# Kernel tuning notes

Measured on AMD Instinct MI355X. Metric: run time of the kernel, lower is better.

Reference implementation:

```python
import jax, jax.numpy as jnp
import numpy as np

EMBED = 1024
HEADS = 16
HEAD_DIM = EMBED // HEADS


def setup_inputs() -> dict:
    key = jax.random.key(0)
    ks = jax.random.split(key, 6)
    N, S = 4, 1024
    query = jax.random.normal(ks[0], (N, S, EMBED), dtype=jnp.float32)
    keys = jax.random.normal(ks[1], (N, S, EMBED), dtype=jnp.float32)
    values = jax.random.normal(ks[2], (N, S, EMBED), dtype=jnp.float32)
    mask = jax.random.randint(ks[3], (N, 1, S, S), 0, 2, dtype=jnp.int32)
    W_out = jax.random.normal(ks[4], (EMBED, EMBED), dtype=jnp.float32) * (1.0 / np.sqrt(EMBED))
    b_out = jax.random.normal(ks[5], (EMBED,), dtype=jnp.float32) * 0.02
    return {"query": query, "keys": keys, "values": values, "mask": mask,
            "W_out": W_out, "b_out": b_out}


def reference(query, keys, values, mask, W_out, b_out):
    N, Q, _ = query.shape
    K = keys.shape[1]
    # NOTE: the torch module never applies its per-head q/k/v Linear layers;
    # only the reshape + attention + fc_out are in the forward path.
    q = query.reshape(N, Q, HEADS, HEAD_DIM)
    k = keys.reshape(N, K, HEADS, HEAD_DIM)
    v = values.reshape(N, K, HEADS, HEAD_DIM)
    # energy: [N, H, Q, K]
    energy = jnp.einsum("bqhd,bkhd->bhqk", q, k)
    energy = jnp.where(mask == 0, jnp.float32(-1e20), energy)
    attn = jax.nn.softmax(energy / jnp.sqrt(jnp.float32(HEAD_DIM)), axis=3)
    out = jnp.einsum("bhqk,bkhd->bqhd", attn, v).reshape(N, Q, HEADS * HEAD_DIM)
    return out @ W_out.T + b_out
```

## Files before the change

### kernel.cpp

```cpp
#include <hip/hip_runtime.h>
#include <math.h>

#define NB 4
#define SL 1024
#define EMB 1024
#define NH 16
#define HD 64
#define QB 128

typedef __attribute__((ext_vector_type(8))) short bf16x8;
typedef __attribute__((ext_vector_type(4))) float f32x4;
typedef __attribute__((ext_vector_type(4))) unsigned u32x4;

static __device__ __forceinline__ unsigned pk2(float a, float b) {
    unsigned x = __float_as_uint(a) + 0x8000u;
    unsigned y = __float_as_uint(b) + 0x8000u;
    return (x >> 16) | (y & 0xFFFF0000u);
}
static __device__ __forceinline__ float exp2_fast(float x) {
    float r; asm("v_exp_f32 %0, %1" : "=v"(r) : "v"(x)); return r;
}
static __device__ __forceinline__ void gload_lds16(const void* g, void* l) {
    __builtin_amdgcn_global_load_lds(
        (const __attribute__((address_space(1))) unsigned int*)g,
        (__attribute__((address_space(3))) unsigned int*)l, 16, 0, 0);
}

#define VMW(n) asm volatile("s_waitcnt vmcnt(" #n ")" ::: "memory")
#define MEMPIN() asm volatile("" ::: "memory")

__global__ __launch_bounds__(256) void prep(
    const float* __restrict__ W, unsigned short* __restrict__ Wb,
    const float* __restrict__ Kf, unsigned short* __restrict__ Kb,
    const float* __restrict__ V, unsigned short* __restrict__ Vt,
    const int* __restrict__ mask, unsigned long long* __restrict__ Mbt,
    const float* __restrict__ Qf, unsigned short* __restrict__ Qb)
{
    __shared__ unsigned short sT[128 * 68];
    const int bid = blockIdx.x, tid = threadIdx.x;

    if (bid < 512) {
        int i = (bid * 256 + tid) * 8;
        float4 f0 = *(const float4*)&W[i];
        float4 f1 = *(const float4*)&W[i + 4];
        uint4 u = { pk2(f0.x,f0.y), pk2(f0.z,f0.w), pk2(f1.x,f1.y), pk2(f1.z,f1.w) };
        *(uint4*)&Wb[i] = u;
    } else if (bid < 2560) {
        int t = bid - 512;
        int b = t >> 9, h = (t >> 5) & 15, k0 = (t & 31) * 32;
        int r = tid >> 3, d = (tid & 7) * 8;
        const float* gp = &Kf[((size_t)(b * SL + k0 + r)) * EMB + h * HD + d];
        float4 f0 = *(const float4*)gp, f1 = *(const float4*)(gp + 4);
        uint4 u = { pk2(f0.x,f0.y), pk2(f0.z,f0.w), pk2(f1.x,f1.y), pk2(f1.z,f1.w) };
        *(uint4*)&Kb[((size_t)((b * NH + h) * SL + k0 + r)) * HD + d] = u;
    } else if (bid < 3072) {
        int t = bid - 2560;
        int bh = t >> 3, kb = t & 7;
        int b = bh >> 4, h = bh & 15;
        int k0 = kb * 128;
        #pragma unroll
        for (int i = 0; i < 4; ++i) {
            int lin = (i * 256 + tid) * 8;
            int r = lin >> 6, d = lin & 63;
            const float* gp = &V[((size_t)(b * SL + k0 + r)) * EMB + h * HD + d];
            float4 f0 = *(const float4*)gp, f1 = *(const float4*)(gp + 4);
            uint2 u0 = { pk2(f0.x,f0.y), pk2(f0.z,f0.w) };
            uint2 u1 = { pk2(f1.x,f1.y), pk2(f1.z,f1.w) };
            *(uint2*)&sT[r * 68 + d]     = u0;
            *(uint2*)&sT[r * 68 + d + 4] = u1;
        }
        __syncthreads();
        #pragma unroll
        for (int p = 0; p < 4; ++p) {
            int d = p * 16 + (tid >> 4);
            int c = tid & 15;
            unsigned v[4];
            #pragma unroll
            for (int j = 0; j < 4; ++j) {
                unsigned lo = sT[(c * 8 + 2 * j) * 68 + d];
                unsigned hi = sT[(c * 8 + 2 * j + 1) * 68 + d];
                v[j] = lo | (hi << 16);
            }
            uint4 u = { v[0], v[1], v[2], v[3] };
            *(uint4*)&Vt[((size_t)(bh * HD + d)) * SL + k0 + c * 8] = u;
        }
    } else if (bid < 7168) {
        int t = bid - 3072;
        int lane = tid & 63;
        #pragma unroll
        for (int r = 0; r < 4; ++r) {
            int wid = (t * 4 + (tid >> 6)) * 4 + r;
            int c = wid & 15, q = (wid >> 4) & 1023, bb = wid >> 14;
            int mv = mask[((size_t)bb * SL + q) * SL + c * 64 + lane];
            unsigned long long bits = __ballot(mv != 0);
            if (lane == 0) Mbt[((size_t)bb * 16 + c) * SL + q] = bits;
        }
    } else {
        int t = bid - 7168;
        int b = t >> 9, h = (t >> 5) & 15, q0 = (t & 31) * 32;
        int r = tid >> 3, d = (tid & 7) * 8;
        const float* gp = &Qf[((size_t)(b * SL + q0 + r)) * EMB + h * HD + d];
        float4 f0 = *(const float4*)gp, f1 = *(const float4*)(gp + 4);
        uint4 u = { pk2(f0.x,f0.y), pk2(f0.z,f0.w), pk2(f1.x,f1.y), pk2(f1.z,f1.w) };
        *(uint4*)&Qb[((size_t)((b * NH + h) * SL + q0 + r)) * HD + d] = u;
    }
}

__global__ __launch_bounds__(256, 2) void attn_mfma(
    const unsigned short* __restrict__ Qb, const unsigned short* __restrict__ Kb,
    const unsigned short* __restrict__ Vt,
    const unsigned long long* __restrict__ Mbt,
    unsigned short* __restrict__ Oa)
{
    const int lin = blockIdx.x;
    const int xcd = lin & 7, slot = lin >> 3;
    const int bh = xcd * 8 + (slot >> 3);
    const int q0 = (slot & 7) * QB;
    const int b = bh >> 4, h = bh & 15;
    const int tid = threadIdx.x;
    const int w = tid >> 6, lane = tid & 63;
    const int m16 = lane & 15, quad = lane >> 4;
    const int lr = lane >> 3, lc = lane & 7;

    __shared__ __align__(16) unsigned short sK[3][64 * 64];
    __shared__ __align__(16) unsigned short sVt[3][64 * 64];

    const size_t vbase = (size_t)(bh * HD) * SL;
    const size_t kbase = (size_t)(bh * SL) * HD;
    const size_t mbase = (size_t)(b * 16) * SL + q0 + w * 32 + m16;
    const size_t qrowb = (size_t)(bh * SL + q0 + w * 32);

    bf16x8 bQ[2][2];
    #pragma unroll
    for (int u = 0; u < 2; ++u)
        #pragma unroll
        for (int hh = 0; hh < 2; ++hh)
            bQ[u][hh] = *(const bf16x8*)&Qb[(qrowb + u * 16 + m16) * HD + hh * 32 + quad * 8];
    MEMPIN();
    unsigned long long mbA0, mbA1, mbB0, mbB1, mbC0 = 0, mbC1 = 0;
    #pragma unroll
    for (int i = 0; i < 2; ++i) {
        int row = w * 16 + i * 8;
        gload_lds16(&Vt[vbase + (size_t)(row + lr) * SL + (lc ^ lr) * 8], &sVt[0][row * 64]);
        gload_lds16(&Kb[kbase + (size_t)(row + lr) * HD + (lc ^ lr) * 8], &sK[0][row * 64]);
    }
    MEMPIN();
    mbA0 = Mbt[mbase];
    mbA1 = Mbt[mbase + 16];
    MEMPIN();
    #pragma unroll
    for (int i = 0; i < 2; ++i) {
        int row = w * 16 + i * 8;
        gload_lds16(&Vt[vbase + (size_t)(row + lr) * SL + 64 + (lc ^ lr) * 8], &sVt[1][row * 64]);
        gload_lds16(&Kb[kbase + (size_t)(64 + row + lr) * HD + (lc ^ lr) * 8], &sK[1][row * 64]);
    }
    MEMPIN();
    mbB0 = Mbt[mbase + SL];
    mbB1 = Mbt[mbase + SL + 16];
    MEMPIN();

    unsigned short* kc = (unsigned short*)sK[0];
    unsigned short* kn = (unsigned short*)sK[1];
    unsigned short* k2 = (unsigned short*)sK[2];
    unsigned short* vc = (unsigned short*)sVt[0];
    unsigned short* vn = (unsigned short*)sVt[1];
    unsigned short* v2 = (unsigned short*)sVt[2];

    f32x4 O[2][4] = {};
    f32x4 lacc[2] = {};
    const float CSC = 0.125f * 1.44269504f;
    const short one_bf = (short)0x3F80;
    const bf16x8 ones = { one_bf, one_bf, one_bf, one_bf, one_bf, one_bf, one_bf, one_bf };

    for (int kt = 0; kt < 16; ++kt) {
        if (kt < 15) { VMW(8); } else { VMW(2); }
        __builtin_amdgcn_s_barrier();
        __builtin_amdgcn_sched_barrier(0);

        if (kt < 14) {
            const int k0n = (kt + 2) * 64;
            #pragma unroll
            for (int i = 0; i < 2; ++i) {
                int row = w * 16 + i * 8;
                gload_lds16(&Vt[vbase + (size_t)(row + lr) * SL + k0n + (lc ^ lr) * 8],
                            &v2[row * 64]);
                gload_lds16(&Kb[kbase + (size_t)(k0n + row + lr) * HD + (lc ^ lr) * 8],
                            &k2[row * 64]);
            }
            MEMPIN();
            mbC0 = Mbt[mbase + (size_t)(kt + 2) * SL];
            mbC1 = Mbt[mbase + (size_t)(kt + 2) * SL + 16];
            MEMPIN();
        }

        f32x4 sc[2][4];
        __builtin_amdgcn_s_setprio(1);
        #pragma unroll
        for (int t = 0; t < 4; ++t) {
            int krow = t * 16 + m16;
            bf16x8 a0 = *(const bf16x8*)&kc[krow * 64 + ((quad ^ (krow & 7)) * 8)];
            bf16x8 a1 = *(const bf16x8*)&kc[krow * 64 + (((4 + quad) ^ (krow & 7)) * 8)];
            f32x4 z = {0.f, 0.f, 0.f, 0.f};
            sc[0][t] = __builtin_amdgcn_mfma_f32_16x16x32_bf16(a0, bQ[0][0], z,        0,0,0);
            sc[0][t] = __builtin_amdgcn_mfma_f32_16x16x32_bf16(a1, bQ[0][1], sc[0][t], 0,0,0);
            sc[1][t] = __builtin_amdgcn_mfma_f32_16x16x32_bf16(a0, bQ[1][0], z,        0,0,0);
            sc[1][t] = __builtin_amdgcn_mfma_f32_16x16x32_bf16(a1, bQ[1][1], sc[1][t], 0,0,0);
        }
        __builtin_amdgcn_s_setprio(0);

        bf16x8 bP[2][2];
        #pragma unroll
        for (int u = 0; u < 2; ++u) {
            unsigned long long mb = u ? mbA1 : mbA0;
            unsigned mlo = (unsigned)mb, mhi = (unsigned)(mb >> 32);
            unsigned s0 = mlo >> (quad * 8);
            unsigned s1 = mhi >> (quad * 8);
            unsigned wt[4][2];
            #pragma unroll
            for (int t = 0; t < 4; ++t) {
                wt[t][0] = pk2(exp2_fast(sc[u][t][0] * CSC), exp2_fast(sc[u][t][1] * CSC));
                wt[t][1] = pk2(exp2_fast(sc[u][t][2] * CSC), exp2_fast(sc[u][t][3] * CSC));
            }
            unsigned g[2][4];
            #pragma unroll
            for (int hh = 0; hh < 2; ++hh)
                #pragma unroll
                for (int p = 0; p < 2; ++p) {
                    unsigned A = wt[2 * hh][p], B = wt[2 * hh + 1][p];
                    asm("v_permlane32_swap_b32 %0, %1" : "+v"(A), "+v"(B));
                    asm("v_permlane16_swap_b32 %0, %1" : "+v"(A), "+v"(B));
                    g[hh][p] = A; g[hh][2 + p] = B;
                }
            #pragma unroll
            for (int hh = 0; hh < 2; ++hh) {
                unsigned sb = hh ? s1 : s0;
                #pragma unroll
                for (int j2 = 0; j2 < 4; ++j2) {
                    unsigned b2 = (sb >> (2 * j2)) & 3u;
                    unsigned am = ((b2 & 1u) ? 0xFFFFu : 0u) | ((b2 & 2u) ? 0xFFFF0000u : 0u);
                    g[hh][j2] &= am;
                }
            }
            u32x4 p0 = { g[0][0], g[0][1], g[0][2], g[0][3] };
            u32x4 p1 = { g[1][0], g[1][1], g[1][2], g[1][3] };
            bP[u][0] = __builtin_bit_cast(bf16x8, p0);
            bP[u][1] = __builtin_bit_cast(bf16x8, p1);
        }

        __builtin_amdgcn_s_setprio(1);
        lacc[0] = __builtin_amdgcn_mfma_f32_16x16x32_bf16(ones, bP[0][0], lacc[0], 0,0,0);
        lacc[0] = __builtin_amdgcn_mfma_f32_16x16x32_bf16(ones, bP[0][1], lacc[0], 0,0,0);
        lacc[1] = __builtin_amdgcn_mfma_f32_16x16x32_bf16(ones, bP[1][0], lacc[1], 0,0,0);
        lacc[1] = __builtin_amdgcn_mfma_f32_16x16x32_bf16(ones, bP[1][1], lacc[1], 0,0,0);

        #pragma unroll
        for (int dt = 0; dt < 4; ++dt) {
            int drow = dt * 16 + m16;
            bf16x8 v0 = *(const bf16x8*)&vc[drow * 64 + ((quad ^ (drow & 7)) * 8)];
            bf16x8 v1 = *(const bf16x8*)&vc[drow * 64 + (((4 + quad) ^ (drow & 7)) * 8)];
            O[0][dt] = __builtin_amdgcn_mfma_f32_16x16x32_bf16(v0, bP[0][0], O[0][dt], 0,0,0);
            O[0][dt] = __builtin_amdgcn_mfma_f32_16x16x32_bf16(v1, bP[0][1], O[0][dt], 0,0,0);
            O[1][dt] = __builtin_amdgcn_mfma_f32_16x16x32_bf16(v0, bP[1][0], O[1][dt], 0,0,0);
            O[1][dt] = __builtin_amdgcn_mfma_f32_16x16x32_bf16(v1, bP[1][1], O[1][dt], 0,0,0);
        }
        __builtin_amdgcn_s_setprio(0);

        unsigned short* tk = kc; kc = kn; kn = k2; k2 = tk;
        unsigned short* tv = vc; vc = vn; vn = v2; v2 = tv;
        mbA0 = mbB0; mbA1 = mbB1; mbB0 = mbC0; mbB1 = mbC1;
    }

    #pragma unroll
    for (int u = 0; u < 2; ++u) {
        float inv = 1.f / lacc[u][0];
        size_t base = ((size_t)(b * SL + q0 + w * 32 + u * 16 + m16)) * EMB + h * HD + quad * 4;
        #pragma unroll
        for (int dt = 0; dt < 4; ++dt) {
            uint2 ow = { pk2(O[u][dt][0] * inv, O[u][dt][1] * inv),
                         pk2(O[u][dt][2] * inv, O[u][dt][3] * inv) };
            *(uint2*)&Oa[base + dt * 16] = ow;
        }
    }
}

__global__ __launch_bounds__(512, 2) void proj_mfma(
    const unsigned short* __restrict__ A, const unsigned short* __restrict__ Wb,
    const float* __restrict__ bias, float* __restrict__ C)
{
    const int n0 = blockIdx.x * 128;
    const int m0 = blockIdx.y * 128;
    const int tid = threadIdx.x;
    const int w = tid >> 6, lane = tid & 63;
    const int m16 = lane & 15, quad = lane >> 4;
    const int lr = lane >> 3, lc = lane & 7;
    const int wm = (w >> 2) * 64, wn = (w & 3) * 32;

    __shared__ __align__(16) unsigned short sA[2][128 * 64];
    __shared__ __align__(16) unsigned short sW[2][128 * 64];

    f32x4 acc[4][2] = {};

    #pragma unroll
    for (int i = 0; i < 2; ++i) {
        int r = w * 16 + i * 8;
        gload_lds16(&A [(size_t)(m0 + r + lr) * EMB + (lc ^ lr) * 8], &sA[0][r * 64]);
        gload_lds16(&Wb[(size_t)(n0 + r + lr) * EMB + (lc ^ lr) * 8], &sW[0][r * 64]);
    }
    __syncthreads();

    for (int it = 0; it < 16; ++it) {
        const int bf = it & 1;
        if (it < 15) {
            int e0 = (it + 1) * 64;
            #pragma unroll
            for (int i = 0; i < 2; ++i) {
                int r = w * 16 + i * 8;
                gload_lds16(&A [(size_t)(m0 + r + lr) * EMB + e0 + (lc ^ lr) * 8], &sA[bf ^ 1][r * 64]);
                gload_lds16(&Wb[(size_t)(n0 + r + lr) * EMB + e0 + (lc ^ lr) * 8], &sW[bf ^ 1][r * 64]);
            }
        }
        #pragma unroll
        for (int hh = 0; hh < 2; ++hh) {
            bf16x8 af[4], bw[2];
            #pragma unroll
            for (int mt = 0; mt < 4; ++mt) {
                int r = wm + mt * 16 + m16;
                af[mt] = *(const bf16x8*)&sA[bf][r * 64 + (((hh * 4 + quad) ^ (r & 7)) * 8)];
            }
            #pragma unroll
            for (int nt = 0; nt < 2; ++nt) {
                int r = wn + nt * 16 + m16;
                bw[nt] = *(const bf16x8*)&sW[bf][r * 64 + (((hh * 4 + quad) ^ (r & 7)) * 8)];
            }
            #pragma unroll
            for (int mt = 0; mt < 4; ++mt)
                #pragma unroll
                for (int nt = 0; nt < 2; ++nt)
                    acc[mt][nt] = __builtin_amdgcn_mfma_f32_16x16x32_bf16(af[mt], bw[nt], acc[mt][nt], 0,0,0);
        }
        __syncthreads();
    }

    #pragma unroll
    for (int nt = 0; nt < 2; ++nt) {
        float bv = bias[n0 + wn + nt * 16 + m16];
        #pragma unroll
        for (int mt = 0; mt < 4; ++mt) {
            size_t row = (size_t)(m0 + wm + mt * 16 + quad * 4);
            #pragma unroll
            for (int rg = 0; rg < 4; ++rg)
                C[(row + rg) * EMB + n0 + wn + nt * 16 + m16] = acc[mt][nt][rg] + bv;
        }
    }
}

extern "C" void kernel_launch(void* const* d_in, const int* in_sizes, int n_in,
                              void* d_out, int out_size, void* d_ws, size_t ws_size,
                              hipStream_t stream) {
    const float* Q    = (const float*)d_in[0];
    const float* K    = (const float*)d_in[1];
    const float* V    = (const float*)d_in[2];
    const int*   mask = (const int*)  d_in[3];
    const float* W    = (const float*)d_in[4];
    const float* bias = (const float*)d_in[5];

    unsigned short* Oa = (unsigned short*)d_ws;
    unsigned short* Wb = Oa + (size_t)NB * SL * EMB;
    unsigned long long* Mbt = (unsigned long long*)(Wb + (size_t)EMB * EMB);
    unsigned short* Vt = (unsigned short*)(Mbt + (size_t)NB * 16 * SL);
    unsigned short* Kb = Vt + (size_t)NB * NH * HD * SL;
    unsigned short* Qb = Kb + (size_t)NB * NH * SL * HD;

    prep<<<9216, 256, 0, stream>>>(W, Wb, K, Kb, V, Vt, mask, Mbt, Q, Qb);
    attn_mfma<<<512, 256, 0, stream>>>(Qb, Kb, Vt, Mbt, Oa);
    proj_mfma<<<dim3(EMB / 128, (NB * SL) / 128), 512, 0, stream>>>(Oa, Wb, bias, (float*)d_out);
}
```

Before: 167.5 us.

## Halve attention query tile and convert Q to bf16 inside attention kernel

The attention kernel now processes 64 query rows per block (16 per wave) instead of 128, doubling the grid to 1024 blocks and raising the occupancy hint to 3 blocks per CU. Q is read directly as fp32 and packed to bf16 in registers, which removes the Q conversion blocks from the prep kernel and the Qb workspace round trip. The trade-off is that each K/V tile loaded into LDS is now reused by half as many query rows, so total K/V traffic doubles. Each wave also has less MFMA work to hide load latency.

```diff
diff --git a/kernel.cpp b/kernel.cpp
--- a/kernel.cpp
+++ b/kernel.cpp
@@ -6,7 +6,7 @@
 #define EMB 1024
 #define NH 16
 #define HD 64
-#define QB 128
+#define QB 64
 
 typedef __attribute__((ext_vector_type(8))) short bf16x8;
 typedef __attribute__((ext_vector_type(4))) float f32x4;
@@ -33,8 +33,7 @@
     const float* __restrict__ W, unsigned short* __restrict__ Wb,
     const float* __restrict__ Kf, unsigned short* __restrict__ Kb,
     const float* __restrict__ V, unsigned short* __restrict__ Vt,
-    const int* __restrict__ mask, unsigned long long* __restrict__ Mbt,
-    const float* __restrict__ Qf, unsigned short* __restrict__ Qb)
+    const int* __restrict__ mask, unsigned long long* __restrict__ Mbt)
 {
     __shared__ unsigned short sT[128 * 68];
     const int bid = blockIdx.x, tid = threadIdx.x;
@@ -84,7 +83,7 @@
             uint4 u = { v[0], v[1], v[2], v[3] };
             *(uint4*)&Vt[((size_t)(bh * HD + d)) * SL + k0 + c * 8] = u;
         }
-    } else if (bid < 7168) {
+    } else {
         int t = bid - 3072;
         int lane = tid & 63;
         #pragma unroll
@@ -95,27 +94,19 @@
             unsigned long long bits = __ballot(mv != 0);
             if (lane == 0) Mbt[((size_t)bb * 16 + c) * SL + q] = bits;
         }
-    } else {
-        int t = bid - 7168;
-        int b = t >> 9, h = (t >> 5) & 15, q0 = (t & 31) * 32;
-        int r = tid >> 3, d = (tid & 7) * 8;
-        const float* gp = &Qf[((size_t)(b * SL + q0 + r)) * EMB + h * HD + d];
-        float4 f0 = *(const float4*)gp, f1 = *(const float4*)(gp + 4);
-        uint4 u = { pk2(f0.x,f0.y), pk2(f0.z,f0.w), pk2(f1.x,f1.y), pk2(f1.z,f1.w) };
-        *(uint4*)&Qb[((size_t)((b * NH + h) * SL + q0 + r)) * HD + d] = u;
-    }
-}
-
-__global__ __launch_bounds__(256, 2) void attn_mfma(
-    const unsigned short* __restrict__ Qb, const unsigned short* __restrict__ Kb,
+    }
+}
+
+__global__ __launch_bounds__(256, 3) void attn_mfma(
+    const float* __restrict__ Q, const unsigned short* __restrict__ Kb,
     const unsigned short* __restrict__ Vt,
     const unsigned long long* __restrict__ Mbt,
     unsigned short* __restrict__ Oa)
 {
     const int lin = blockIdx.x;
     const int xcd = lin & 7, slot = lin >> 3;
-    const int bh = xcd * 8 + (slot >> 3);
-    const int q0 = (slot & 7) * QB;
+    const int bh = xcd * 8 + (slot >> 4);
+    const int q0 = (slot & 15) * QB;
     const int b = bh >> 4, h = bh & 15;
     const int tid = threadIdx.x;
     const int w = tid >> 6, lane = tid & 63;
@@ -127,17 +118,20 @@
 
     const size_t vbase = (size_t)(bh * HD) * SL;
     const size_t kbase = (size_t)(bh * SL) * HD;
-    const size_t mbase = (size_t)(b * 16) * SL + q0 + w * 32 + m16;
-    const size_t qrowb = (size_t)(bh * SL + q0 + w * 32);
-
-    bf16x8 bQ[2][2];
-    #pragma unroll
-    for (int u = 0; u < 2; ++u)
-        #pragma unroll
-        for (int hh = 0; hh < 2; ++hh)
-            bQ[u][hh] = *(const bf16x8*)&Qb[(qrowb + u * 16 + m16) * HD + hh * 32 + quad * 8];
-    MEMPIN();
-    unsigned long long mbA0, mbA1, mbB0, mbB1, mbC0 = 0, mbC1 = 0;
+    const size_t mbase = (size_t)(b * 16) * SL + q0 + w * 16 + m16;
+
+    bf16x8 bQ[2];
+    {
+        const float* qp = &Q[((size_t)(b * SL + q0 + w * 16 + m16)) * EMB + h * HD + quad * 8];
+        float4 f0 = *(const float4*)qp,        f1 = *(const float4*)(qp + 4);
+        float4 f2 = *(const float4*)(qp + 32), f3 = *(const float4*)(qp + 36);
+        u32x4 u0 = { pk2(f0.x,f0.y), pk2(f0.z,f0.w), pk2(f1.x,f1.y), pk2(f1.z,f1.w) };
+        u32x4 u1 = { pk2(f2.x,f2.y), pk2(f2.z,f2.w), pk2(f3.x,f3.y), pk2(f3.z,f3.w) };
+        bQ[0] = __builtin_bit_cast(bf16x8, u0);
+        bQ[1] = __builtin_bit_cast(bf16x8, u1);
+    }
+    MEMPIN();
+    unsigned long long mbA, mbB, mbC = 0;
     #pragma unroll
     for (int i = 0; i < 2; ++i) {
         int row = w * 16 + i * 8;
@@ -145,8 +139,7 @@
         gload_lds16(&Kb[kbase + (size_t)(row + lr) * HD + (lc ^ lr) * 8], &sK[0][row * 64]);
     }
     MEMPIN();
-    mbA0 = Mbt[mbase];
-    mbA1 = Mbt[mbase + 16];
+    mbA = Mbt[mbase];
     MEMPIN();
     #pragma unroll
     for (int i = 0; i < 2; ++i) {
@@ -155,8 +148,7 @@
         gload_lds16(&Kb[kbase + (size_t)(64 + row + lr) * HD + (lc ^ lr) * 8], &sK[1][row * 64]);
     }
     MEMPIN();
-    mbB0 = Mbt[mbase + SL];
-    mbB1 = Mbt[mbase + SL + 16];
+    mbB = Mbt[mbase + SL];
     MEMPIN();
 
     unsigned short* kc = (unsigned short*)sK[0];
@@ -166,14 +158,14 @@
     unsigned short* vn = (unsigned short*)sVt[1];
     unsigned short* v2 = (unsigned short*)sVt[2];
 
-    f32x4 O[2][4] = {};
-    f32x4 lacc[2] = {};
+    f32x4 O[4] = {};
+    f32x4 lacc = {};
     const float CSC = 0.125f * 1.44269504f;
     const short one_bf = (short)0x3F80;
     const bf16x8 ones = { one_bf, one_bf, one_bf, one_bf, one_bf, one_bf, one_bf, one_bf };
 
     for (int kt = 0; kt < 16; ++kt) {
-        if (kt < 15) { VMW(8); } else { VMW(2); }
+        if (kt < 15) { VMW(5); } else { VMW(1); }
         __builtin_amdgcn_s_barrier();
         __builtin_amdgcn_sched_barrier(0);
 
@@ -188,12 +180,11 @@
                             &k2[row * 64]);
             }
             MEMPIN();
-            mbC0 = Mbt[mbase + (size_t)(kt + 2) * SL];
-            mbC1 = Mbt[mbase + (size_t)(kt + 2) * SL + 16];
+            mbC = Mbt[mbase + (size_t)(kt + 2) * SL];
             MEMPIN();
         }
 
-        f32x4 sc[2][4];
+        f32x4 sc[4];
         __builtin_amdgcn_s_setprio(1);
         #pragma unroll
         for (int t = 0; t < 4; ++t) {
@@ -201,25 +192,21 @@
             bf16x8 a0 = *(const bf16x8*)&kc[krow * 64 + ((quad ^ (krow & 7)) * 8)];
             bf16x8 a1 = *(const bf16x8*)&kc[krow * 64 + (((4 + quad) ^ (krow & 7)) * 8)];
             f32x4 z = {0.f, 0.f, 0.f, 0.f};
-            sc[0][t] = __builtin_amdgcn_mfma_f32_16x16x32_bf16(a0, bQ[0][0], z,        0,0,0);
-            sc[0][t] = __builtin_amdgcn_mfma_f32_16x16x32_bf16(a1, bQ[0][1], sc[0][t], 0,0,0);
-            sc[1][t] = __builtin_amdgcn_mfma_f32_16x16x32_bf16(a0, bQ[1][0], z,        0,0,0);
-            sc[1][t] = __builtin_amdgcn_mfma_f32_16x16x32_bf16(a1, bQ[1][1], sc[1][t], 0,0,0);
+            sc[t] = __builtin_amdgcn_mfma_f32_16x16x32_bf16(a0, bQ[0], z,     0,0,0);
+            sc[t] = __builtin_amdgcn_mfma_f32_16x16x32_bf16(a1, bQ[1], sc[t], 0,0,0);
         }
         __builtin_amdgcn_s_setprio(0);
 
-        bf16x8 bP[2][2];
-        #pragma unroll
-        for (int u = 0; u < 2; ++u) {
-            unsigned long long mb = u ? mbA1 : mbA0;
-            unsigned mlo = (unsigned)mb, mhi = (unsigned)(mb >> 32);
+        bf16x8 bP[2];
+        {
+            unsigned mlo = (unsigned)mbA, mhi = (unsigned)(mbA >> 32);
             unsigned s0 = mlo >> (quad * 8);
             unsigned s1 = mhi >> (quad * 8);
             unsigned wt[4][2];
             #pragma unroll
             for (int t = 0; t < 4; ++t) {
-                wt[t][0] = pk2(exp2_fast(sc[u][t][0] * CSC), exp2_fast(sc[u][t][1] * CSC));
-                wt[t][1] = pk2(exp2_fast(sc[u][t][2] * CSC), exp2_fast(sc[u][t][3] * CSC));
+                wt[t][0] = pk2(exp2_fast(sc[t][0] * CSC), exp2_fast(sc[t][1] * CSC));
+                wt[t][1] = pk2(exp2_fast(sc[t][2] * CSC), exp2_fast(sc[t][3] * CSC));
             }
             unsigned g[2][4];
             #pragma unroll
@@ -243,41 +230,36 @@
             }
             u32x4 p0 = { g[0][0], g[0][1], g[0][2], g[0][3] };
             u32x4 p1 = { g[1][0], g[1][1], g[1][2], g[1][3] };
-            bP[u][0] = __builtin_bit_cast(bf16x8, p0);
-            bP[u][1] = __builtin_bit_cast(bf16x8, p1);
+            bP[0] = __builtin_bit_cast(bf16x8, p0);
+            bP[1] = __builtin_bit_cast(bf16x8, p1);
         }
 
         __builtin_amdgcn_s_setprio(1);
-        lacc[0] = __builtin_amdgcn_mfma_f32_16x16x32_bf16(ones, bP[0][0], lacc[0], 0,0,0);
-        lacc[0] = __builtin_amdgcn_mfma_f32_16x16x32_bf16(ones, bP[0][1], lacc[0], 0,0,0);
-        lacc[1] = __builtin_amdgcn_mfma_f32_16x16x32_bf16(ones, bP[1][0], lacc[1], 0,0,0);
-        lacc[1] = __builtin_amdgcn_mfma_f32_16x16x32_bf16(ones, bP[1][1], lacc[1], 0,0,0);
+        lacc = __builtin_amdgcn_mfma_f32_16x16x32_bf16(ones, bP[0], lacc, 0,0,0);
+        lacc = __builtin_amdgcn_mfma_f32_16x16x32_bf16(ones, bP[1], lacc, 0,0,0);
 
         #pragma unroll
         for (int dt = 0; dt < 4; ++dt) {
             int drow = dt * 16 + m16;
             bf16x8 v0 = *(const bf16x8*)&vc[drow * 64 + ((quad ^ (drow & 7)) * 8)];
             bf16x8 v1 = *(const bf16x8*)&vc[drow * 64 + (((4 + quad) ^ (drow & 7)) * 8)];
-            O[0][dt] = __builtin_amdgcn_mfma_f32_16x16x32_bf16(v0, bP[0][0], O[0][dt], 0,0,0);
-            O[0][dt] = __builtin_amdgcn_mfma_f32_16x16x32_bf16(v1, bP[0][1], O[0][dt], 0,0,0);
-            O[1][dt] = __builtin_amdgcn_mfma_f32_16x16x32_bf16(v0, bP[1][0], O[1][dt], 0,0,0);
-            O[1][dt] = __builtin_amdgcn_mfma_f32_16x16x32_bf16(v1, bP[1][1], O[1][dt], 0,0,0);
+            O[dt] = __builtin_amdgcn_mfma_f32_16x16x32_bf16(v0, bP[0], O[dt], 0,0,0);
+            O[dt] = __builtin_amdgcn_mfma_f32_16x16x32_bf16(v1, bP[1], O[dt], 0,0,0);
         }
         __builtin_amdgcn_s_setprio(0);
 
         unsigned short* tk = kc; kc = kn; kn = k2; k2 = tk;
         unsigned short* tv = vc; vc = vn; vn = v2; v2 = tv;
-        mbA0 = mbB0; mbA1 = mbB1; mbB0 = mbC0; mbB1 = mbC1;
-    }
-
-    #pragma unroll
-    for (int u = 0; u < 2; ++u) {
-        float inv = 1.f / lacc[u][0];
-        size_t base = ((size_t)(b * SL + q0 + w * 32 + u * 16 + m16)) * EMB + h * HD + quad * 4;
+        mbA = mbB; mbB = mbC;
+    }
+
+    {
+        float inv = 1.f / lacc[0];
+        size_t base = ((size_t)(b * SL + q0 + w * 16 + m16)) * EMB + h * HD + quad * 4;
         #pragma unroll
         for (int dt = 0; dt < 4; ++dt) {
-            uint2 ow = { pk2(O[u][dt][0] * inv, O[u][dt][1] * inv),
-                         pk2(O[u][dt][2] * inv, O[u][dt][3] * inv) };
+            uint2 ow = { pk2(O[dt][0] * inv, O[dt][1] * inv),
+                         pk2(O[dt][2] * inv, O[dt][3] * inv) };
             *(uint2*)&Oa[base + dt * 16] = ow;
         }
     }
@@ -369,9 +351,8 @@
     unsigned long long* Mbt = (unsigned long long*)(Wb + (size_t)EMB * EMB);
     unsigned short* Vt = (unsigned short*)(Mbt + (size_t)NB * 16 * SL);
     unsigned short* Kb = Vt + (size_t)NB * NH * HD * SL;
-    unsigned short* Qb = Kb + (size_t)NB * NH * SL * HD;
-
-    prep<<<9216, 256, 0, stream>>>(W, Wb, K, Kb, V, Vt, mask, Mbt, Q, Qb);
-    attn_mfma<<<512, 256, 0, stream>>>(Qb, Kb, Vt, Mbt, Oa);
+
+    prep<<<7168, 256, 0, stream>>>(W, Wb, K, Kb, V, Vt, mask, Mbt);
+    attn_mfma<<<1024, 256, 0, stream>>>(Q, Kb, Vt, Mbt, Oa);
     proj_mfma<<<dim3(EMB / 128, (NB * SL) / 128), 512, 0, stream>>>(Oa, Wb, bias, (float*)d_out);
 }
```

New measurement: 169.6 us. About the same (+1.2%).

## Split key range across two wave groups, fuse Q conversion into attention

Applied to the files above, without the earlier changes.

The attention kernel now uses 512 threads. Two groups of four waves each process alternating 64-key tiles, and their partial O and row-sum accumulators are combined through LDS at the end. Q is loaded as fp32 and converted to bf16 inside the attention kernel, so the Q pass in prep is gone, and the softmax scale is folded into K during prep. Packing uses the hardware v_cvt_pk_bf16_f32 and a cheaper mask expansion. The pipeline is now a 4-slot buffer with a full vmcnt(0) wait every iteration. That wait and the final reduction could cut latency hiding, but the split gives more waves per block.

```diff
diff --git a/kernel.cpp b/kernel.cpp
--- a/kernel.cpp
+++ b/kernel.cpp
@@ -20,6 +20,9 @@
 static __device__ __forceinline__ float exp2_fast(float x) {
     float r; asm("v_exp_f32 %0, %1" : "=v"(r) : "v"(x)); return r;
 }
+static __device__ __forceinline__ unsigned cvtpk(float a, float b) {
+    unsigned r; asm("v_cvt_pk_bf16_f32 %0, %1, %2" : "=v"(r) : "v"(a), "v"(b)); return r;
+}
 static __device__ __forceinline__ void gload_lds16(const void* g, void* l) {
     __builtin_amdgcn_global_load_lds(
         (const __attribute__((address_space(1))) unsigned int*)g,
@@ -33,11 +36,11 @@
     const float* __restrict__ W, unsigned short* __restrict__ Wb,
     const float* __restrict__ Kf, unsigned short* __restrict__ Kb,
     const float* __restrict__ V, unsigned short* __restrict__ Vt,
-    const int* __restrict__ mask, unsigned long long* __restrict__ Mbt,
-    const float* __restrict__ Qf, unsigned short* __restrict__ Qb)
+    const int* __restrict__ mask, unsigned long long* __restrict__ Mbt)
 {
     __shared__ unsigned short sT[128 * 68];
     const int bid = blockIdx.x, tid = threadIdx.x;
+    const float CSC = 0.125f * 1.44269504f;
 
     if (bid < 512) {
         int i = (bid * 256 + tid) * 8;
@@ -51,7 +54,8 @@
         int r = tid >> 3, d = (tid & 7) * 8;
         const float* gp = &Kf[((size_t)(b * SL + k0 + r)) * EMB + h * HD + d];
         float4 f0 = *(const float4*)gp, f1 = *(const float4*)(gp + 4);
-        uint4 u = { pk2(f0.x,f0.y), pk2(f0.z,f0.w), pk2(f1.x,f1.y), pk2(f1.z,f1.w) };
+        uint4 u = { pk2(f0.x*CSC,f0.y*CSC), pk2(f0.z*CSC,f0.w*CSC),
+                    pk2(f1.x*CSC,f1.y*CSC), pk2(f1.z*CSC,f1.w*CSC) };
         *(uint4*)&Kb[((size_t)((b * NH + h) * SL + k0 + r)) * HD + d] = u;
     } else if (bid < 3072) {
         int t = bid - 2560;
@@ -84,7 +88,7 @@
             uint4 u = { v[0], v[1], v[2], v[3] };
             *(uint4*)&Vt[((size_t)(bh * HD + d)) * SL + k0 + c * 8] = u;
         }
-    } else if (bid < 7168) {
+    } else {
         int t = bid - 3072;
         int lane = tid & 63;
         #pragma unroll
@@ -95,19 +99,11 @@
             unsigned long long bits = __ballot(mv != 0);
             if (lane == 0) Mbt[((size_t)bb * 16 + c) * SL + q] = bits;
         }
-    } else {
-        int t = bid - 7168;
-        int b = t >> 9, h = (t >> 5) & 15, q0 = (t & 31) * 32;
-        int r = tid >> 3, d = (tid & 7) * 8;
-        const float* gp = &Qf[((size_t)(b * SL + q0 + r)) * EMB + h * HD + d];
-        float4 f0 = *(const float4*)gp, f1 = *(const float4*)(gp + 4);
-        uint4 u = { pk2(f0.x,f0.y), pk2(f0.z,f0.w), pk2(f1.x,f1.y), pk2(f1.z,f1.w) };
-        *(uint4*)&Qb[((size_t)((b * NH + h) * SL + q0 + r)) * HD + d] = u;
-    }
-}
-
-__global__ __launch_bounds__(256, 2) void attn_mfma(
-    const unsigned short* __restrict__ Qb, const unsigned short* __restrict__ Kb,
+    }
+}
+
+__global__ __launch_bounds__(512, 4) void attn_mfma(
+    const float* __restrict__ Q, const unsigned short* __restrict__ Kb,
     const unsigned short* __restrict__ Vt,
     const unsigned long long* __restrict__ Mbt,
     unsigned short* __restrict__ Oa)
@@ -121,105 +117,107 @@
     const int w = tid >> 6, lane = tid & 63;
     const int m16 = lane & 15, quad = lane >> 4;
     const int lr = lane >> 3, lc = lane & 7;
-
-    __shared__ __align__(16) unsigned short sK[3][64 * 64];
-    __shared__ __align__(16) unsigned short sVt[3][64 * 64];
+    const int grp = w >> 2;
+    const int wq = w & 3;
+    const int srow = w * 8;
+
+    __shared__ __align__(16) unsigned short sAll[32768];
+    unsigned short* sKb = sAll;
+    unsigned short* sVb = sAll + 16384;
 
     const size_t vbase = (size_t)(bh * HD) * SL;
     const size_t kbase = (size_t)(bh * SL) * HD;
-    const size_t mbase = (size_t)(b * 16) * SL + q0 + w * 32 + m16;
-    const size_t qrowb = (size_t)(bh * SL + q0 + w * 32);
+    const unsigned long long* Mp = Mbt + (size_t)(b * 16) * SL + q0 + wq * 32 + m16;
+
+    float4 qf[2][4];
+    #pragma unroll
+    for (int u = 0; u < 2; ++u) {
+        const float* qp = &Q[((size_t)(b * SL + q0 + wq * 32 + u * 16 + m16)) * EMB + h * HD + quad * 8];
+        qf[u][0] = *(const float4*)qp;        qf[u][1] = *(const float4*)(qp + 4);
+        qf[u][2] = *(const float4*)(qp + 32); qf[u][3] = *(const float4*)(qp + 36);
+    }
+    MEMPIN();
+    #pragma unroll
+    for (int t2 = 0; t2 < 2; ++t2) {
+        gload_lds16(&Vt[vbase + (size_t)(srow + lr) * SL + t2 * 64 + (lc ^ lr) * 8],
+                    &sVb[t2 * 4096 + srow * 64]);
+        gload_lds16(&Kb[kbase + (size_t)(t2 * 64 + srow + lr) * HD + (lc ^ lr) * 8],
+                    &sKb[t2 * 4096 + srow * 64]);
+    }
+    MEMPIN();
+    unsigned long long mbC0 = Mp[(size_t)grp * SL];
+    unsigned long long mbC1 = Mp[(size_t)grp * SL + 16];
+    unsigned long long mbN0 = 0, mbN1 = 0;
+    MEMPIN();
 
     bf16x8 bQ[2][2];
     #pragma unroll
-    for (int u = 0; u < 2; ++u)
-        #pragma unroll
-        for (int hh = 0; hh < 2; ++hh)
-            bQ[u][hh] = *(const bf16x8*)&Qb[(qrowb + u * 16 + m16) * HD + hh * 32 + quad * 8];
-    MEMPIN();
-    unsigned long long mbA0, mbA1, mbB0, mbB1, mbC0 = 0, mbC1 = 0;
-    #pragma unroll
-    for (int i = 0; i < 2; ++i) {
-        int row = w * 16 + i * 8;
-        gload_lds16(&Vt[vbase + (size_t)(row + lr) * SL + (lc ^ lr) * 8], &sVt[0][row * 64]);
-        gload_lds16(&Kb[kbase + (size_t)(row + lr) * HD + (lc ^ lr) * 8], &sK[0][row * 64]);
-    }
-    MEMPIN();
-    mbA0 = Mbt[mbase];
-    mbA1 = Mbt[mbase + 16];
-    MEMPIN();
-    #pragma unroll
-    for (int i = 0; i < 2; ++i) {
-        int row = w * 16 + i * 8;
-        gload_lds16(&Vt[vbase + (size_t)(row + lr) * SL + 64 + (lc ^ lr) * 8], &sVt[1][row * 64]);
-        gload_lds16(&Kb[kbase + (size_t)(64 + row + lr) * HD + (lc ^ lr) * 8], &sK[1][row * 64]);
-    }
-    MEMPIN();
-    mbB0 = Mbt[mbase + SL];
-    mbB1 = Mbt[mbase + SL + 16];
-    MEMPIN();
-
-    unsigned short* kc = (unsigned short*)sK[0];
-    unsigned short* kn = (unsigned short*)sK[1];
-    unsigned short* k2 = (unsigned short*)sK[2];
-    unsigned short* vc = (unsigned short*)sVt[0];
-    unsigned short* vn = (unsigned short*)sVt[1];
-    unsigned short* v2 = (unsigned short*)sVt[2];
+    for (int u = 0; u < 2; ++u) {
+        u32x4 u0 = { pk2(qf[u][0].x,qf[u][0].y), pk2(qf[u][0].z,qf[u][0].w),
+                     pk2(qf[u][1].x,qf[u][1].y), pk2(qf[u][1].z,qf[u][1].w) };
+        u32x4 u1 = { pk2(qf[u][2].x,qf[u][2].y), pk2(qf[u][2].z,qf[u][2].w),
+                     pk2(qf[u][3].x,qf[u][3].y), pk2(qf[u][3].z,qf[u][3].w) };
+        bQ[u][0] = __builtin_bit_cast(bf16x8, u0);
+        bQ[u][1] = __builtin_bit_cast(bf16x8, u1);
+    }
 
     f32x4 O[2][4] = {};
     f32x4 lacc[2] = {};
-    const float CSC = 0.125f * 1.44269504f;
     const short one_bf = (short)0x3F80;
     const bf16x8 ones = { one_bf, one_bf, one_bf, one_bf, one_bf, one_bf, one_bf, one_bf };
 
-    for (int kt = 0; kt < 16; ++kt) {
-        if (kt < 15) { VMW(8); } else { VMW(2); }
+    for (int i = 0; i < 8; ++i) {
+        VMW(0);
         __builtin_amdgcn_s_barrier();
         __builtin_amdgcn_sched_barrier(0);
 
-        if (kt < 14) {
-            const int k0n = (kt + 2) * 64;
-            #pragma unroll
-            for (int i = 0; i < 2; ++i) {
-                int row = w * 16 + i * 8;
-                gload_lds16(&Vt[vbase + (size_t)(row + lr) * SL + k0n + (lc ^ lr) * 8],
-                            &v2[row * 64]);
-                gload_lds16(&Kb[kbase + (size_t)(k0n + row + lr) * HD + (lc ^ lr) * 8],
-                            &k2[row * 64]);
-            }
+        const int t = 2 * i + grp;
+        if (i < 7) {
+            const int tE = 2 * i + 2;
+            const int bE = tE & 3, bO = (tE + 1) & 3;
+            gload_lds16(&Vt[vbase + (size_t)(srow + lr) * SL + tE * 64 + (lc ^ lr) * 8],
+                        &sVb[bE * 4096 + srow * 64]);
+            gload_lds16(&Kb[kbase + (size_t)(tE * 64 + srow + lr) * HD + (lc ^ lr) * 8],
+                        &sKb[bE * 4096 + srow * 64]);
+            gload_lds16(&Vt[vbase + (size_t)(srow + lr) * SL + (tE + 1) * 64 + (lc ^ lr) * 8],
+                        &sVb[bO * 4096 + srow * 64]);
+            gload_lds16(&Kb[kbase + (size_t)((tE + 1) * 64 + srow + lr) * HD + (lc ^ lr) * 8],
+                        &sKb[bO * 4096 + srow * 64]);
             MEMPIN();
-            mbC0 = Mbt[mbase + (size_t)(kt + 2) * SL];
-            mbC1 = Mbt[mbase + (size_t)(kt + 2) * SL + 16];
+            mbN0 = Mp[(size_t)(t + 2) * SL];
+            mbN1 = Mp[(size_t)(t + 2) * SL + 16];
             MEMPIN();
         }
+
+        const unsigned short* kc = &sKb[(t & 3) * 4096];
+        const unsigned short* vc = &sVb[(t & 3) * 4096];
 
         f32x4 sc[2][4];
         __builtin_amdgcn_s_setprio(1);
         #pragma unroll
-        for (int t = 0; t < 4; ++t) {
-            int krow = t * 16 + m16;
+        for (int t4 = 0; t4 < 4; ++t4) {
+            int krow = t4 * 16 + m16;
             bf16x8 a0 = *(const bf16x8*)&kc[krow * 64 + ((quad ^ (krow & 7)) * 8)];
             bf16x8 a1 = *(const bf16x8*)&kc[krow * 64 + (((4 + quad) ^ (krow & 7)) * 8)];
             f32x4 z = {0.f, 0.f, 0.f, 0.f};
-            sc[0][t] = __builtin_amdgcn_mfma_f32_16x16x32_bf16(a0, bQ[0][0], z,        0,0,0);
-            sc[0][t] = __builtin_amdgcn_mfma_f32_16x16x32_bf16(a1, bQ[0][1], sc[0][t], 0,0,0);
-            sc[1][t] = __builtin_amdgcn_mfma_f32_16x16x32_bf16(a0, bQ[1][0], z,        0,0,0);
-            sc[1][t] = __builtin_amdgcn_mfma_f32_16x16x32_bf16(a1, bQ[1][1], sc[1][t], 0,0,0);
+            sc[0][t4] = __builtin_amdgcn_mfma_f32_16x16x32_bf16(a0, bQ[0][0], z,         0,0,0);
+            sc[0][t4] = __builtin_amdgcn_mfma_f32_16x16x32_bf16(a1, bQ[0][1], sc[0][t4], 0,0,0);
+            sc[1][t4] = __builtin_amdgcn_mfma_f32_16x16x32_bf16(a0, bQ[1][0], z,         0,0,0);
+            sc[1][t4] = __builtin_amdgcn_mfma_f32_16x16x32_bf16(a1, bQ[1][1], sc[1][t4], 0,0,0);
         }
         __builtin_amdgcn_s_setprio(0);
 
         bf16x8 bP[2][2];
         #pragma unroll
         for (int u = 0; u < 2; ++u) {
-            unsigned long long mb = u ? mbA1 : mbA0;
-            unsigned mlo = (unsigned)mb, mhi = (unsigned)(mb >> 32);
-            unsigned s0 = mlo >> (quad * 8);
-            unsigned s1 = mhi >> (quad * 8);
+            unsigned long long mb = u ? mbC1 : mbC0;
+            unsigned s0 = ((unsigned)mb) >> (quad * 8);
+            unsigned s1 = ((unsigned)(mb >> 32)) >> (quad * 8);
             unsigned wt[4][2];
             #pragma unroll
-            for (int t = 0; t < 4; ++t) {
-                wt[t][0] = pk2(exp2_fast(sc[u][t][0] * CSC), exp2_fast(sc[u][t][1] * CSC));
-                wt[t][1] = pk2(exp2_fast(sc[u][t][2] * CSC), exp2_fast(sc[u][t][3] * CSC));
+            for (int t4 = 0; t4 < 4; ++t4) {
+                wt[t4][0] = cvtpk(exp2_fast(sc[u][t4][0]), exp2_fast(sc[u][t4][1]));
+                wt[t4][1] = cvtpk(exp2_fast(sc[u][t4][2]), exp2_fast(sc[u][t4][3]));
             }
             unsigned g[2][4];
             #pragma unroll
@@ -236,9 +234,9 @@
                 unsigned sb = hh ? s1 : s0;
                 #pragma unroll
                 for (int j2 = 0; j2 < 4; ++j2) {
-                    unsigned b2 = (sb >> (2 * j2)) & 3u;
-                    unsigned am = ((b2 & 1u) ? 0xFFFFu : 0u) | ((b2 & 2u) ? 0xFFFF0000u : 0u);
-                    g[hh][j2] &= am;
+                    unsigned mlo = (unsigned)(((int)(sb << (31 - 2 * j2))) >> 31);
+                    unsigned mhi = (unsigned)(((int)(sb << (30 - 2 * j2))) >> 31);
+                    g[hh][j2] &= (mlo & 0xFFFFu) | (mhi & 0xFFFF0000u);
                 }
             }
             u32x4 p0 = { g[0][0], g[0][1], g[0][2], g[0][3] };
@@ -265,20 +263,37 @@
         }
         __builtin_amdgcn_s_setprio(0);
 
-        unsigned short* tk = kc; kc = kn; kn = k2; k2 = tk;
-        unsigned short* tv = vc; vc = vn; vn = v2; v2 = tv;
-        mbA0 = mbB0; mbA1 = mbB1; mbB0 = mbC0; mbB1 = mbC1;
-    }
-
-    #pragma unroll
-    for (int u = 0; u < 2; ++u) {
-        float inv = 1.f / lacc[u][0];
-        size_t base = ((size_t)(b * SL + q0 + w * 32 + u * 16 + m16)) * EMB + h * HD + quad * 4;
-        #pragma unroll
-        for (int dt = 0; dt < 4; ++dt) {
-            uint2 ow = { pk2(O[u][dt][0] * inv, O[u][dt][1] * inv),
-                         pk2(O[u][dt][2] * inv, O[u][dt][3] * inv) };
-            *(uint2*)&Oa[base + dt * 16] = ow;
+        mbC0 = mbN0; mbC1 = mbN1;
+    }
+
+    __syncthreads();
+    float* sM = (float*)sAll;
+    if (grp == 1) {
+        #pragma unroll
+        for (int u = 0; u < 2; ++u)
+            #pragma unroll
+            for (int dt = 0; dt < 4; ++dt)
+                *(f32x4*)&sM[((u * 4 + dt) * 256 + wq * 64 + lane) * 4] = O[u][dt];
+        sM[8192 + (wq * 64 + lane) * 2 + 0] = lacc[0][0];
+        sM[8192 + (wq * 64 + lane) * 2 + 1] = lacc[1][0];
+    }
+    __syncthreads();
+    if (grp == 0) {
+        float l[2];
+        l[0] = lacc[0][0] + sM[8192 + (wq * 64 + lane) * 2 + 0];
+        l[1] = lacc[1][0] + sM[8192 + (wq * 64 + lane) * 2 + 1];
+        #pragma unroll
+        for (int u = 0; u < 2; ++u) {
+            float inv = 1.f / l[u];
+            size_t base = ((size_t)(b * SL + q0 + wq * 32 + u * 16 + m16)) * EMB + h * HD + quad * 4;
+            #pragma unroll
+            for (int dt = 0; dt < 4; ++dt) {
+                f32x4 part = *(const f32x4*)&sM[((u * 4 + dt) * 256 + wq * 64 + lane) * 4];
+                f32x4 o = O[u][dt] + part;
+                uint2 ow = { cvtpk(o[0] * inv, o[1] * inv),
+                             cvtpk(o[2] * inv, o[3] * inv) };
+                *(uint2*)&Oa[base + dt * 16] = ow;
+            }
         }
     }
 }
@@ -369,9 +384,8 @@
     unsigned long long* Mbt = (unsigned long long*)(Wb + (size_t)EMB * EMB);
     unsigned short* Vt = (unsigned short*)(Mbt + (size_t)NB * 16 * SL);
     unsigned short* Kb = Vt + (size_t)NB * NH * HD * SL;
-    unsigned short* Qb = Kb + (size_t)NB * NH * SL * HD;
-
-    prep<<<9216, 256, 0, stream>>>(W, Wb, K, Kb, V, Vt, mask, Mbt, Q, Qb);
-    attn_mfma<<<512, 256, 0, stream>>>(Qb, Kb, Vt, Mbt, Oa);
+
+    prep<<<7168, 256, 0, stream>>>(W, Wb, K, Kb, V, Vt, mask, Mbt);
+    attn_mfma<<<512, 512, 0, stream>>>(Q, Kb, Vt, Mbt, Oa);
     proj_mfma<<<dim3(EMB / 128, (NB * SL) / 128), 512, 0, stream>>>(Oa, Wb, bias, (float*)d_out);
 }
```

Result: faster. 160.0 us (-4.5%).
